# Kernel optimization log

Measured on AMD Instinct MI355X. Metric: run time of the kernel, lower is better.

## Reference

```python
import jax, jax.numpy as jnp
import numpy as np

BLOCK_SIZE = 64
SPARSITY_RATIO = 0.5


def _band_mask(seq_len, block_size, sparsity_ratio):
    # Block (i, j) is computed iff max(0, i-w) <= j < min(nb, i+w), w = int(nb*ratio).
    nb = seq_len // block_size
    w = int(nb * sparsity_ratio)
    ib = jnp.arange(nb)
    bm = (ib[None, :] >= ib[:, None] - w) & (ib[None, :] < ib[:, None] + w)  # [nb, nb]
    return jnp.repeat(jnp.repeat(bm, block_size, axis=0), block_size, axis=1)  # [S, S]


def setup_inputs() -> dict:
    key = jax.random.key(0)
    kq, kk, kv = jax.random.split(key, 3)
    B, S, D = 4, 4096, 128
    return {
        "query": jax.random.normal(kq, (B, S, D), dtype=jnp.float32),
        "key": jax.random.normal(kk, (B, S, D), dtype=jnp.float32),
        "value": jax.random.normal(kv, (B, S, D), dtype=jnp.float32),
    }


def reference(query, key, value):
    B, S, D = query.shape
    mask = _band_mask(S, BLOCK_SIZE, SPARSITY_RATIO)  # [S, S] bool
    scores = jnp.einsum('bqd,bkd->bqk', query, key)  # [B, S, S]
    # Outside-band entries stay exactly 0 (NOT -inf) — matches torch.zeros init.
    scores = jnp.where(mask[None, :, :], scores, jnp.zeros((), scores.dtype))
    probs = jax.nn.softmax(scores, axis=-1)
    return jnp.matmul(probs, value)  # [B, S, D]
```

## Files before the change

kernel.cpp:

```cpp
#include <hip/hip_runtime.h>


typedef _Float16 f16;
typedef __attribute__((ext_vector_type(8))) _Float16 f16x8;
typedef __attribute__((ext_vector_type(4))) _Float16 f16x4;
typedef __attribute__((ext_vector_type(4))) float f32x4;

#define MFMA16(a, b, c) __builtin_amdgcn_mfma_f32_16x16x32_f16((a), (b), (c), 0, 0, 0)

#define BATCH 4
#define SEQ   4096
#define DIM   128
#define NB    64
#define WBAND 32
#define LOG2E 1.44269504088896f
#define DTHR  8.0f

#define KTILE 16384
#define VTILE 16384
#define TSTR  72

#define CHUNKS 4
#define PART_STRIDE 16896

__device__ __forceinline__ void gl16(const char* g, char* l) {
  __builtin_amdgcn_global_load_lds(
      (const __attribute__((address_space(1))) void*)g,
      (__attribute__((address_space(3))) void*)l, 16, 0, 0);
}

__global__ __launch_bounds__(256) void convert_kernel(
    const float* __restrict__ K, const float* __restrict__ V,
    f16* __restrict__ KT, f16* __restrict__ VT, float* __restrict__ BS) {
  __shared__ f16 T[128 * TSTR];
  const int blk = blockIdx.x;
  const int b = blk >> 6, jb = blk & 63;
  const int s0 = jb * 64;
  const int t = threadIdx.x;
  char* ktile = (char*)KT + (size_t)blk * KTILE;
  char* vtile = (char*)VT + (size_t)blk * VTILE;

#pragma unroll
  for (int i = 0; i < 4; ++i) {
    int idx = t + i * 256;
    int row = idx >> 4;
    int c = idx & 15;
    const float* src = K + ((size_t)(b * SEQ + s0 + row)) * DIM + c * 8;
    float4 a = *(const float4*)src;
    float4 d = *(const float4*)(src + 4);
    f16x8 h = {(f16)a.x, (f16)a.y, (f16)a.z, (f16)a.w,
               (f16)d.x, (f16)d.y, (f16)d.z, (f16)d.w};
    *(f16x8*)(ktile + row * 256 + ((c ^ (row & 15)) * 16)) = h;
  }

#pragma unroll
  for (int i = 0; i < 8; ++i) {
    int idx = t + i * 256;
    int row = idx >> 5;
    int c4 = (idx & 31) * 4;
    float4 v = *(const float4*)(V + (size_t)(b * SEQ + s0 + row) * DIM + c4);
    T[(c4 + 0) * TSTR + row] = (f16)v.x;
    T[(c4 + 1) * TSTR + row] = (f16)v.y;
    T[(c4 + 2) * TSTR + row] = (f16)v.z;
    T[(c4 + 3) * TSTR + row] = (f16)v.w;
  }
  __syncthreads();

#pragma unroll
  for (int i = 0; i < 4; ++i) {
    int idx = t + i * 256;
    int d = idx >> 3;
    int c = idx & 7;
    f16x8 val = *(const f16x8*)(T + d * TSTR + c * 8);
    *(f16x8*)(vtile + d * 128 + ((c ^ (d & 7)) * 16)) = val;
  }

  if (t < 128) {
    float s = 0.f;
    for (int k = 0; k < 64; ++k) s += (float)T[t * TSTR + k];
    BS[(b * NB + jb) * DIM + t] = s;
  }
}

__global__ __launch_bounds__(256, 4) void attn_kernel(
    const float* __restrict__ Q, const f16* __restrict__ KT,
    const f16* __restrict__ VT, char* __restrict__ PART) {
  __shared__ __align__(16) char smem[40960];

  const int id = blockIdx.x;
  const int lin = (id & 7) * 128 + (id >> 3);
  const int ck = lin & 3;
  const int ib = (lin >> 2) & 63;
  const int b = lin >> 8;

  const int t = threadIdx.x;
  const int w = t >> 6, l = t & 63, lg = l >> 4, ll = l & 15;

  const int jlo = max(0, ib - WBAND);
  const int jhi = min(NB, ib + WBAND);
  const int n = jhi - jlo;
  const int c = (n + 3) >> 2;
  const int j0 = jlo + ck * c;
  const int nloc = min(c, jhi - j0);
  const int q0 = ib * 64;

  f16x8 qf[4];
  {
    const float* qrow = Q + ((size_t)(b * SEQ + q0 + w * 16 + ll)) * DIM;
#pragma unroll
    for (int ks = 0; ks < 4; ++ks) {
      int d0 = ks * 32 + lg * 8;
      float4 a = *(const float4*)(qrow + d0);
      float4 cc = *(const float4*)(qrow + d0 + 4);
      float vv[8] = {a.x, a.y, a.z, a.w, cc.x, cc.y, cc.z, cc.w};
#pragma unroll
      for (int e = 0; e < 8; ++e) qf[ks][e] = (f16)(vv[e] * LOG2E);
    }
  }

  float m2 = 0.f;
  float ell = 0.f;
  f32x4 o[8];
#pragma unroll
  for (int nt = 0; nt < 8; ++nt) o[nt] = (f32x4){0.f, 0.f, 0.f, 0.f};

  f16* Pw = (f16*)(smem + 32768 + w * 2048);

  auto stage = [&](int jb) {
    const char* kg = (const char*)KT + ((size_t)(b * NB + jb)) * KTILE + t * 16;
    const char* vg = (const char*)VT + ((size_t)(b * NB + jb)) * VTILE + t * 16;
#pragma unroll
    for (int i = 0; i < 4; ++i) gl16(kg + i * 4096, smem + t * 16 + i * 4096);
#pragma unroll
    for (int i = 0; i < 4; ++i) gl16(vg + i * 4096, smem + 16384 + t * 16 + i * 4096);
  };

  stage(j0);
  __syncthreads();

  for (int tt = 0; tt < nloc; ++tt) {
    const char* kb = smem;
    const char* vb = smem + 16384;

    f32x4 sacc[4];
#pragma unroll
    for (int jt = 0; jt < 4; ++jt) sacc[jt] = (f32x4){0.f, 0.f, 0.f, 0.f};
    __builtin_amdgcn_s_setprio(1);
#pragma unroll
    for (int ks = 0; ks < 4; ++ks) {
#pragma unroll
      for (int jt = 0; jt < 4; ++jt) {
        int row = jt * 16 + ll;
        f16x8 kf = *(const f16x8*)(kb + row * 256 + (((ks * 4 + lg) ^ ll) * 16));
        sacc[jt] = MFMA16(kf, qf[ks], sacc[jt]);
      }
    }
    __builtin_amdgcn_s_setprio(0);

    float vm = sacc[0][0];
#pragma unroll
    for (int jt = 0; jt < 4; ++jt)
#pragma unroll
      for (int r = 0; r < 4; ++r) vm = fmaxf(vm, sacc[jt][r]);
    vm = fmaxf(vm, __shfl_xor(vm, 16));
    vm = fmaxf(vm, __shfl_xor(vm, 32));

    if (__any(vm - m2 > DTHR)) {
      float nm = fmaxf(m2, vm);
      float scl = __builtin_amdgcn_exp2f(m2 - nm);
      m2 = nm;
      ell *= scl;
      float sb[4];
#pragma unroll
      for (int r = 0; r < 4; ++r) sb[r] = __shfl(scl, lg * 4 + r);
#pragma unroll
      for (int nt = 0; nt < 8; ++nt)
#pragma unroll
        for (int r = 0; r < 4; ++r) o[nt][r] *= sb[r];
    }

    float rsum = 0.f;
#pragma unroll
    for (int jt = 0; jt < 4; ++jt) {
      f16x4 pk;
#pragma unroll
      for (int r = 0; r < 4; ++r) {
        float p = __builtin_amdgcn_exp2f(sacc[jt][r] - m2);
        rsum += p;
        pk[r] = (f16)p;
      }
      *(f16x4*)(Pw + ll * 64 + ((jt * 16 + lg * 4) ^ ((ll & 7) << 3))) = pk;
    }
    ell += rsum;

    __builtin_amdgcn_s_setprio(1);
#pragma unroll
    for (int ks2 = 0; ks2 < 2; ++ks2) {
      f16x8 pa = *(const f16x8*)(Pw + ll * 64 + ((ks2 * 32 + lg * 8) ^ ((ll & 7) << 3)));
#pragma unroll
      for (int nt = 0; nt < 8; ++nt) {
        int d = nt * 16 + ll;
        f16x8 vbf = *(const f16x8*)(vb + d * 128 + ((((ks2 * 4 + lg) ^ (ll & 7)) * 16)));
        o[nt] = MFMA16(pa, vbf, o[nt]);
      }
    }
    __builtin_amdgcn_s_setprio(0);

    __syncthreads();
    if (tt + 1 < nloc) stage(j0 + tt + 1);
    __syncthreads();
  }

  ell += __shfl_xor(ell, 16);
  ell += __shfl_xor(ell, 32);

  char* pb = PART + ((size_t)((b * NB + ib) * CHUNKS + ck)) * PART_STRIDE;
  f16* oc = (f16*)(pb + (w * 64 + l) * 64);
#pragma unroll
  for (int g = 0; g < 4; ++g) {
    f16x8 hh;
#pragma unroll
    for (int r = 0; r < 4; ++r) {
      hh[r] = (f16)o[g * 2][r];
      hh[4 + r] = (f16)o[g * 2 + 1][r];
    }
    *(f16x8*)(oc + g * 8) = hh;
  }
  if (lg == 0) {
    *(float2*)(pb + 16384 + (w * 16 + ll) * 8) = make_float2(m2, ell);
  }
}

__global__ __launch_bounds__(256) void merge_kernel(
    const char* __restrict__ PART, const float* __restrict__ BS,
    float* __restrict__ Out) {
  __shared__ float VoutS[DIM];
  __shared__ float mlS[CHUNKS][64][2];

  const int id = blockIdx.x;
  const int lin = (id & 7) * 32 + (id >> 3);
  const int b = lin >> 6, ib = lin & 63;
  const int t = threadIdx.x;
  const int w = t >> 6, l = t & 63, lg = l >> 4, ll = l & 15;

  const int jlo = max(0, ib - WBAND);
  const int jhi = min(NB, ib + WBAND);
  const int n = jhi - jlo;
  const float cnt_out = (float)(SEQ - n * 64);

  if (t < DIM) {
    float s = 0.f;
    for (int j = 0; j < jlo; ++j) s += BS[(b * NB + j) * DIM + t];
    for (int j = jhi; j < NB; ++j) s += BS[(b * NB + j) * DIM + t];
    VoutS[t] = s;
  }
  const char* pbase = PART + (size_t)((b * NB + ib) * CHUNKS) * PART_STRIDE;
  {
    int k = t >> 6, row = t & 63;
    *(float2*)&mlS[k][row][0] =
        *(const float2*)(pbase + (size_t)k * PART_STRIDE + 16384 + row * 8);
  }
  __syncthreads();

  float aw[4][CHUNKS], en[4], inv[4];
#pragma unroll
  for (int r = 0; r < 4; ++r) {
    int row = w * 16 + lg * 4 + r;
    float M = mlS[0][row][0];
#pragma unroll
    for (int k = 1; k < CHUNKS; ++k) M = fmaxf(M, mlS[k][row][0]);
    en[r] = __builtin_amdgcn_exp2f(-M);
    float den = cnt_out * en[r];
#pragma unroll
    for (int k = 0; k < CHUNKS; ++k) {
      aw[r][k] = __builtin_amdgcn_exp2f(mlS[k][row][0] - M);
      den += aw[r][k] * mlS[k][row][1];
    }
    inv[r] = 1.f / den;
  }

  float acc[8][4];
#pragma unroll
  for (int nt = 0; nt < 8; ++nt)
#pragma unroll
    for (int r = 0; r < 4; ++r) acc[nt][r] = 0.f;

#pragma unroll
  for (int k = 0; k < CHUNKS; ++k) {
    const f16* oc = (const f16*)(pbase + (size_t)k * PART_STRIDE + (w * 64 + l) * 64);
#pragma unroll
    for (int g = 0; g < 4; ++g) {
      f16x8 h = *(const f16x8*)(oc + g * 8);
#pragma unroll
      for (int r = 0; r < 4; ++r) {
        acc[g * 2][r] += aw[r][k] * (float)h[r];
        acc[g * 2 + 1][r] += aw[r][k] * (float)h[4 + r];
      }
    }
  }

  const int q0 = ib * 64;
#pragma unroll
  for (int nt = 0; nt < 8; ++nt) {
    int col = nt * 16 + ll;
    float vout = VoutS[col];
#pragma unroll
    for (int r = 0; r < 4; ++r) {
      int row = w * 16 + lg * 4 + r;
      Out[((size_t)(b * SEQ + q0 + row)) * DIM + col] =
          (acc[nt][r] + en[r] * vout) * inv[r];
    }
  }
}

extern "C" void kernel_launch(void* const* d_in, const int* in_sizes, int n_in,
                              void* d_out, int out_size, void* d_ws, size_t ws_size,
                              hipStream_t stream) {
  const float* Q = (const float*)d_in[0];
  const float* K = (const float*)d_in[1];
  const float* V = (const float*)d_in[2];
  float* Out = (float*)d_out;

  char* ws = (char*)d_ws;
  f16* KTg = (f16*)ws;
  f16* VTg = (f16*)(ws + (size_t)BATCH * NB * KTILE);
  float* BS = (float*)(ws + 2 * (size_t)BATCH * NB * KTILE);
  char* PART = ws + 2 * (size_t)BATCH * NB * KTILE + (size_t)BATCH * NB * DIM * 4;

  convert_kernel<<<dim3(BATCH * NB), 256, 0, stream>>>(K, V, KTg, VTg, BS);
  attn_kernel<<<dim3(BATCH * NB * CHUNKS), 256, 0, stream>>>(Q, KTg, VTg, PART);
  merge_kernel<<<dim3(BATCH * NB), 256, 0, stream>>>(PART, BS, Out);
}
```

Before: 64.88 us.

## Process query-block pairs per workgroup to share K/V tiles, split into eight chunks

Each attention workgroup now handles two adjacent 64-row query blocks. Each wave computes 32 query rows against every staged K/V tile and skips tiles outside its own band, so each K/V tile load serves twice as many queries and global/LDS traffic per output drops. The key range is split into eight chunks to keep the grid at the same size, and the merge kernel is updated for the new partial layout. In exchange, LDS grows to 48KB, occupancy is lowered to three blocks per SIMD group, registers per wave roughly double, and the merge has more partials to combine.

```diff
diff --git a/kernel.cpp b/kernel.cpp
--- a/kernel.cpp
+++ b/kernel.cpp
@@ -20,7 +20,7 @@
 #define VTILE 16384
 #define TSTR  72
 
-#define CHUNKS 4
+#define CHUNKS 8
 #define PART_STRIDE 16896
 
 __device__ __forceinline__ void gl16(const char* g, char* l) {
@@ -82,31 +82,36 @@
   }
 }
 
-__global__ __launch_bounds__(256, 4) void attn_kernel(
+__global__ __launch_bounds__(256, 3) void attn_kernel(
     const float* __restrict__ Q, const f16* __restrict__ KT,
     const f16* __restrict__ VT, char* __restrict__ PART) {
-  __shared__ __align__(16) char smem[40960];
+  __shared__ __align__(16) char smem[49152];
 
   const int id = blockIdx.x;
   const int lin = (id & 7) * 128 + (id >> 3);
-  const int ck = lin & 3;
-  const int ib = (lin >> 2) & 63;
-  const int b = lin >> 8;
+  const int ck = lin & 7;
+  const int pair = lin >> 3;
+  const int b = pair >> 5, p = pair & 31;
 
   const int t = threadIdx.x;
   const int w = t >> 6, l = t & 63, lg = l >> 4, ll = l & 15;
-
-  const int jlo = max(0, ib - WBAND);
-  const int jhi = min(NB, ib + WBAND);
-  const int n = jhi - jlo;
-  const int c = (n + 3) >> 2;
-  const int j0 = jlo + ck * c;
-  const int nloc = min(c, jhi - j0);
-  const int q0 = ib * 64;
-
-  f16x8 qf[4];
-  {
-    const float* qrow = Q + ((size_t)(b * SEQ + q0 + w * 16 + ll)) * DIM;
+  const int half = w >> 1, qh = w & 1;
+  const int myib = p * 2 + half;
+
+  const int jloU = max(0, p * 2 - WBAND);
+  const int jhiU = min(NB, p * 2 + 1 + WBAND);
+  const int lenU = jhiU - jloU;
+  const int c = (lenU + CHUNKS - 1) >> 3;
+  const int j0 = jloU + ck * c;
+  const int nloc = min(c, jhiU - j0);
+  const int mylo = max(0, myib - WBAND);
+  const int myhi = min(NB, myib + WBAND);
+
+  f16x8 qf[2][4];
+#pragma unroll
+  for (int s = 0; s < 2; ++s) {
+    const float* qrow =
+        Q + ((size_t)(b * SEQ + myib * 64 + qh * 32 + s * 16 + ll)) * DIM;
 #pragma unroll
     for (int ks = 0; ks < 4; ++ks) {
       int d0 = ks * 32 + lg * 8;
@@ -114,17 +119,21 @@
       float4 cc = *(const float4*)(qrow + d0 + 4);
       float vv[8] = {a.x, a.y, a.z, a.w, cc.x, cc.y, cc.z, cc.w};
 #pragma unroll
-      for (int e = 0; e < 8; ++e) qf[ks][e] = (f16)(vv[e] * LOG2E);
-    }
-  }
-
-  float m2 = 0.f;
-  float ell = 0.f;
-  f32x4 o[8];
-#pragma unroll
-  for (int nt = 0; nt < 8; ++nt) o[nt] = (f32x4){0.f, 0.f, 0.f, 0.f};
-
-  f16* Pw = (f16*)(smem + 32768 + w * 2048);
+      for (int e = 0; e < 8; ++e) qf[s][ks][e] = (f16)(vv[e] * LOG2E);
+    }
+  }
+
+  float m2[2] = {0.f, 0.f};
+  float ell[2] = {0.f, 0.f};
+  f32x4 o[2][8];
+#pragma unroll
+  for (int s = 0; s < 2; ++s)
+#pragma unroll
+    for (int nt = 0; nt < 8; ++nt) o[s][nt] = (f32x4){0.f, 0.f, 0.f, 0.f};
+
+  f16* Pw = (f16*)(smem + 32768 + w * 4096);
+  const char* kb = smem;
+  const char* vb = smem + 16384;
 
   auto stage = [&](int jb) {
     const char* kg = (const char*)KT + ((size_t)(b * NB + jb)) * KTILE + t * 16;
@@ -135,99 +144,118 @@
     for (int i = 0; i < 4; ++i) gl16(vg + i * 4096, smem + 16384 + t * 16 + i * 4096);
   };
 
-  stage(j0);
-  __syncthreads();
-
-  for (int tt = 0; tt < nloc; ++tt) {
-    const char* kb = smem;
-    const char* vb = smem + 16384;
-
-    f32x4 sacc[4];
-#pragma unroll
-    for (int jt = 0; jt < 4; ++jt) sacc[jt] = (f32x4){0.f, 0.f, 0.f, 0.f};
-    __builtin_amdgcn_s_setprio(1);
-#pragma unroll
-    for (int ks = 0; ks < 4; ++ks) {
-#pragma unroll
-      for (int jt = 0; jt < 4; ++jt) {
-        int row = jt * 16 + ll;
-        f16x8 kf = *(const f16x8*)(kb + row * 256 + (((ks * 4 + lg) ^ ll) * 16));
-        sacc[jt] = MFMA16(kf, qf[ks], sacc[jt]);
+  if (nloc > 0) {
+    stage(j0);
+    __syncthreads();
+
+    for (int tt = 0; tt < nloc; ++tt) {
+      const int j = j0 + tt;
+      const bool act = (j >= mylo) && (j < myhi);
+      if (act) {
+        f32x4 sacc[2][4];
+#pragma unroll
+        for (int s = 0; s < 2; ++s)
+#pragma unroll
+          for (int jt = 0; jt < 4; ++jt) sacc[s][jt] = (f32x4){0.f, 0.f, 0.f, 0.f};
+        __builtin_amdgcn_s_setprio(1);
+#pragma unroll
+        for (int ks = 0; ks < 4; ++ks) {
+#pragma unroll
+          for (int jt = 0; jt < 4; ++jt) {
+            int row = jt * 16 + ll;
+            f16x8 kf = *(const f16x8*)(kb + row * 256 + (((ks * 4 + lg) ^ ll) * 16));
+            sacc[0][jt] = MFMA16(kf, qf[0][ks], sacc[0][jt]);
+            sacc[1][jt] = MFMA16(kf, qf[1][ks], sacc[1][jt]);
+          }
+        }
+        __builtin_amdgcn_s_setprio(0);
+
+#pragma unroll
+        for (int s = 0; s < 2; ++s) {
+          float vm = sacc[s][0][0];
+#pragma unroll
+          for (int jt = 0; jt < 4; ++jt)
+#pragma unroll
+            for (int r = 0; r < 4; ++r) vm = fmaxf(vm, sacc[s][jt][r]);
+          vm = fmaxf(vm, __shfl_xor(vm, 16));
+          vm = fmaxf(vm, __shfl_xor(vm, 32));
+
+          if (__any(vm - m2[s] > DTHR)) {
+            float nm = fmaxf(m2[s], vm);
+            float scl = __builtin_amdgcn_exp2f(m2[s] - nm);
+            m2[s] = nm;
+            ell[s] *= scl;
+            float sb[4];
+#pragma unroll
+            for (int r = 0; r < 4; ++r) sb[r] = __shfl(scl, lg * 4 + r);
+#pragma unroll
+            for (int nt = 0; nt < 8; ++nt)
+#pragma unroll
+              for (int r = 0; r < 4; ++r) o[s][nt][r] *= sb[r];
+          }
+
+          float rsum = 0.f;
+#pragma unroll
+          for (int jt = 0; jt < 4; ++jt) {
+            f16x4 pk;
+#pragma unroll
+            for (int r = 0; r < 4; ++r) {
+              float pv = __builtin_amdgcn_exp2f(sacc[s][jt][r] - m2[s]);
+              rsum += pv;
+              pk[r] = (f16)pv;
+            }
+            *(f16x4*)(Pw + s * 1024 + ll * 64 +
+                      ((jt * 16 + lg * 4) ^ ((ll & 7) << 3))) = pk;
+          }
+          ell[s] += rsum;
+        }
+
+        __builtin_amdgcn_s_setprio(1);
+#pragma unroll
+        for (int ks2 = 0; ks2 < 2; ++ks2) {
+          int pcol = (ks2 * 32 + lg * 8) ^ ((ll & 7) << 3);
+          f16x8 pa0 = *(const f16x8*)(Pw + ll * 64 + pcol);
+          f16x8 pa1 = *(const f16x8*)(Pw + 1024 + ll * 64 + pcol);
+#pragma unroll
+          for (int nt = 0; nt < 8; ++nt) {
+            int d = nt * 16 + ll;
+            f16x8 vbf = *(const f16x8*)(vb + d * 128 + (((ks2 * 4 + lg) ^ (ll & 7)) * 16));
+            o[0][nt] = MFMA16(pa0, vbf, o[0][nt]);
+            o[1][nt] = MFMA16(pa1, vbf, o[1][nt]);
+          }
+        }
+        __builtin_amdgcn_s_setprio(0);
       }
-    }
-    __builtin_amdgcn_s_setprio(0);
-
-    float vm = sacc[0][0];
-#pragma unroll
-    for (int jt = 0; jt < 4; ++jt)
-#pragma unroll
-      for (int r = 0; r < 4; ++r) vm = fmaxf(vm, sacc[jt][r]);
-    vm = fmaxf(vm, __shfl_xor(vm, 16));
-    vm = fmaxf(vm, __shfl_xor(vm, 32));
-
-    if (__any(vm - m2 > DTHR)) {
-      float nm = fmaxf(m2, vm);
-      float scl = __builtin_amdgcn_exp2f(m2 - nm);
-      m2 = nm;
-      ell *= scl;
-      float sb[4];
-#pragma unroll
-      for (int r = 0; r < 4; ++r) sb[r] = __shfl(scl, lg * 4 + r);
-#pragma unroll
-      for (int nt = 0; nt < 8; ++nt)
-#pragma unroll
-        for (int r = 0; r < 4; ++r) o[nt][r] *= sb[r];
-    }
-
-    float rsum = 0.f;
-#pragma unroll
-    for (int jt = 0; jt < 4; ++jt) {
-      f16x4 pk;
+      __syncthreads();
+      if (tt + 1 < nloc) stage(j0 + tt + 1);
+      __syncthreads();
+    }
+  }
+
+#pragma unroll
+  for (int s = 0; s < 2; ++s) {
+    ell[s] += __shfl_xor(ell[s], 16);
+    ell[s] += __shfl_xor(ell[s], 32);
+  }
+
+  char* pb = PART + ((size_t)((pair * CHUNKS + ck) * 2 + half)) * PART_STRIDE;
+#pragma unroll
+  for (int s = 0; s < 2; ++s)
+#pragma unroll
+    for (int g = 0; g < 4; ++g) {
+      f16x8 hh;
 #pragma unroll
       for (int r = 0; r < 4; ++r) {
-        float p = __builtin_amdgcn_exp2f(sacc[jt][r] - m2);
-        rsum += p;
-        pk[r] = (f16)p;
+        hh[r] = (f16)o[s][2 * g][r];
+        hh[4 + r] = (f16)o[s][2 * g + 1][r];
       }
-      *(f16x4*)(Pw + ll * 64 + ((jt * 16 + lg * 4) ^ ((ll & 7) << 3))) = pk;
-    }
-    ell += rsum;
-
-    __builtin_amdgcn_s_setprio(1);
-#pragma unroll
-    for (int ks2 = 0; ks2 < 2; ++ks2) {
-      f16x8 pa = *(const f16x8*)(Pw + ll * 64 + ((ks2 * 32 + lg * 8) ^ ((ll & 7) << 3)));
-#pragma unroll
-      for (int nt = 0; nt < 8; ++nt) {
-        int d = nt * 16 + ll;
-        f16x8 vbf = *(const f16x8*)(vb + d * 128 + ((((ks2 * 4 + lg) ^ (ll & 7)) * 16)));
-        o[nt] = MFMA16(pa, vbf, o[nt]);
-      }
-    }
-    __builtin_amdgcn_s_setprio(0);
-
-    __syncthreads();
-    if (tt + 1 < nloc) stage(j0 + tt + 1);
-    __syncthreads();
-  }
-
-  ell += __shfl_xor(ell, 16);
-  ell += __shfl_xor(ell, 32);
-
-  char* pb = PART + ((size_t)((b * NB + ib) * CHUNKS + ck)) * PART_STRIDE;
-  f16* oc = (f16*)(pb + (w * 64 + l) * 64);
-#pragma unroll
-  for (int g = 0; g < 4; ++g) {
-    f16x8 hh;
-#pragma unroll
-    for (int r = 0; r < 4; ++r) {
-      hh[r] = (f16)o[g * 2][r];
-      hh[4 + r] = (f16)o[g * 2 + 1][r];
-    }
-    *(f16x8*)(oc + g * 8) = hh;
-  }
+      *(f16x8*)(pb + qh * 8192 + ((s * 4 + g) * 64 + l) * 16) = hh;
+    }
   if (lg == 0) {
-    *(float2*)(pb + 16384 + (w * 16 + ll) * 8) = make_float2(m2, ell);
+#pragma unroll
+    for (int s = 0; s < 2; ++s)
+      *(float2*)(pb + 16384 + (qh * 32 + s * 16 + ll) * 8) =
+          make_float2(m2[s], ell[s]);
   }
 }
 
@@ -239,14 +267,16 @@
 
   const int id = blockIdx.x;
   const int lin = (id & 7) * 32 + (id >> 3);
-  const int b = lin >> 6, ib = lin & 63;
+  const int pair = lin >> 1, half = lin & 1;
+  const int b = pair >> 5;
+  const int ib = (pair & 31) * 2 + half;
   const int t = threadIdx.x;
-  const int w = t >> 6, l = t & 63, lg = l >> 4, ll = l & 15;
+  const int l = t & 63, lg = (t >> 4) & 3, ll = t & 15;
+  const int sub = (t >> 6) & 1, qh = t >> 7;
 
   const int jlo = max(0, ib - WBAND);
   const int jhi = min(NB, ib + WBAND);
-  const int n = jhi - jlo;
-  const float cnt_out = (float)(SEQ - n * 64);
+  const float cnt_out = (float)(SEQ - (jhi - jlo) * 64);
 
   if (t < DIM) {
     float s = 0.f;
@@ -254,18 +284,19 @@
     for (int j = jhi; j < NB; ++j) s += BS[(b * NB + j) * DIM + t];
     VoutS[t] = s;
   }
-  const char* pbase = PART + (size_t)((b * NB + ib) * CHUNKS) * PART_STRIDE;
-  {
-    int k = t >> 6, row = t & 63;
-    *(float2*)&mlS[k][row][0] =
-        *(const float2*)(pbase + (size_t)k * PART_STRIDE + 16384 + row * 8);
+
+  const size_t pb0 = ((size_t)(pair * CHUNKS * 2 + half)) * PART_STRIDE;
+  for (int i = t; i < CHUNKS * 64; i += 256) {
+    int k = i >> 6, row = i & 63;
+    *(float2*)&mlS[k][row][0] = *(const float2*)(
+        PART + pb0 + (size_t)k * 2 * PART_STRIDE + 16384 + row * 8);
   }
   __syncthreads();
 
   float aw[4][CHUNKS], en[4], inv[4];
 #pragma unroll
   for (int r = 0; r < 4; ++r) {
-    int row = w * 16 + lg * 4 + r;
+    int row = qh * 32 + sub * 16 + lg * 4 + r;
     float M = mlS[0][row][0];
 #pragma unroll
     for (int k = 1; k < CHUNKS; ++k) M = fmaxf(M, mlS[k][row][0]);
@@ -285,16 +316,15 @@
 #pragma unroll
     for (int r = 0; r < 4; ++r) acc[nt][r] = 0.f;
 
-#pragma unroll
   for (int k = 0; k < CHUNKS; ++k) {
-    const f16* oc = (const f16*)(pbase + (size_t)k * PART_STRIDE + (w * 64 + l) * 64);
+    const char* oc = PART + pb0 + (size_t)k * 2 * PART_STRIDE + qh * 8192;
 #pragma unroll
     for (int g = 0; g < 4; ++g) {
-      f16x8 h = *(const f16x8*)(oc + g * 8);
+      f16x8 h = *(const f16x8*)(oc + ((sub * 4 + g) * 64 + l) * 16);
 #pragma unroll
       for (int r = 0; r < 4; ++r) {
-        acc[g * 2][r] += aw[r][k] * (float)h[r];
-        acc[g * 2 + 1][r] += aw[r][k] * (float)h[4 + r];
+        acc[2 * g][r] += aw[r][k] * (float)h[r];
+        acc[2 * g + 1][r] += aw[r][k] * (float)h[4 + r];
       }
     }
   }
@@ -306,7 +336,7 @@
     float vout = VoutS[col];
 #pragma unroll
     for (int r = 0; r < 4; ++r) {
-      int row = w * 16 + lg * 4 + r;
+      int row = qh * 32 + sub * 16 + lg * 4 + r;
       Out[((size_t)(b * SEQ + q0 + row)) * DIM + col] =
           (acc[nt][r] + en[r] * vout) * inv[r];
     }
@@ -328,6 +358,6 @@
   char* PART = ws + 2 * (size_t)BATCH * NB * KTILE + (size_t)BATCH * NB * DIM * 4;
 
   convert_kernel<<<dim3(BATCH * NB), 256, 0, stream>>>(K, V, KTg, VTg, BS);
-  attn_kernel<<<dim3(BATCH * NB * CHUNKS), 256, 0, stream>>>(Q, KTg, VTg, PART);
+  attn_kernel<<<dim3(BATCH * NB / 2 * CHUNKS), 256, 0, stream>>>(Q, KTg, VTg, PART);
   merge_kernel<<<dim3(BATCH * NB), 256, 0, stream>>>(PART, BS, Out);
 }
```

Measured after the change: 65.14 us. No clear change (+0.4%).
